# Kernel optimization log

Measured on AMD Instinct MI355X. Metric: run time of the kernel, lower is better.

The kernel has to match this reference:

```python
import jax, jax.numpy as jnp
import numpy as np

B, N, C, H = 32, 197, 768, 12
D = C // H  # head dim = 64


def setup_inputs() -> dict:
    key = jax.random.key(0)
    ks = jax.random.split(key, 5)
    std = 0.02
    x = jax.random.normal(ks[0], (B, N, C), dtype=jnp.float32)
    w_qkv = jax.random.normal(ks[1], (C, 3 * C), dtype=jnp.float32) * std
    w_proj = jax.random.normal(ks[2], (C, C), dtype=jnp.float32) * std
    b_proj = jnp.zeros((C,), dtype=jnp.float32)
    # 1x1 convs over the head axis of the attention map (Conv2d(H,H,1,bias=False))
    w_conv_l = jax.random.normal(ks[3], (H, H), dtype=jnp.float32) * std + jnp.eye(H, dtype=jnp.float32)
    w_conv_w = jax.random.normal(ks[4], (H, H), dtype=jnp.float32) * std + jnp.eye(H, dtype=jnp.float32)
    return {"x": x, "w_qkv": w_qkv, "w_proj": w_proj, "b_proj": b_proj,
            "w_conv_l": w_conv_l, "w_conv_w": w_conv_w}


def reference(x, w_qkv, w_proj, b_proj, w_conv_l, w_conv_w):
    b, n, c = x.shape
    h, d = H, c // H
    scale = d ** (-0.5)
    qkv = (x @ w_qkv).reshape(b, n, 3, h, d).transpose(2, 0, 3, 1, 4)  # [3,B,H,N,D]
    q, k, v = qkv[0], qkv[1], qkv[2]
    # value_map branch (control_output.need_value_map=True)
    value_map = jax.nn.softmax(jnp.einsum('bhnd,bhmd->bhnm', v, v) * scale, axis=-1)
    # scaled QK^T
    attn = jnp.einsum('bhnd,bhmd->bhnm', q * scale, k)  # [B,H,N,N]
    attention_scores = attn  # need_attn_score=True (captured pre-conv)
    # conv_l: 1x1 conv mixing heads
    attn = jnp.einsum('oh,bhnm->bonm', w_conv_l, attn)
    attention_probs = jax.nn.softmax(attn, axis=-1)  # need_attn_prob=True
    # conv_w: 1x1 conv mixing heads on the probabilities
    attn_w = jnp.einsum('oh,bhnm->bonm', w_conv_w, attention_probs)
    out = jnp.einsum('bhnm,bhmd->bhnd', attn_w, v)  # [B,H,N,D]
    out = out.transpose(0, 2, 1, 3).reshape(b, n, c)
    attention_output = out @ w_proj + b_proj
    return attention_output, attention_scores, attention_probs, value_map
```

## Files before the change

### kernel.cpp

```cpp
#include <hip/hip_runtime.h>
#include <cmath>

#define B_ 32
#define N_ 197
#define C_ 768
#define H_ 12
#define D_ 64
#define M_ (B_*N_)
#define MPAD_ 6400
#define K3_ (3*C_)
#define NN_ (N_*N_)
#define BH_ (B_*H_)
#define NP_ 208
#define KP_ 224
#define SCALE 0.125f

typedef __bf16 bf16x8 __attribute__((ext_vector_type(8)));
typedef __bf16 bf16x4 __attribute__((ext_vector_type(4)));
typedef float  f32x4  __attribute__((ext_vector_type(4)));

__device__ __forceinline__ void gl_lds16(const void* g, void* l) {
    __builtin_amdgcn_global_load_lds(
        (const __attribute__((address_space(1))) void*)g,
        (__attribute__((address_space(3))) void*)l,
        16, 0, 0);
}

__global__ __launch_bounds__(256) void cast_x_kernel(const float* __restrict__ X,
        __bf16* __restrict__ Xb) {
    const long long i = ((long long)blockIdx.x * 256 + threadIdx.x) * 4;
    if (i >= (long long)MPAD_ * 768) return;
    bf16x4 o;
    if (i < (long long)M_ * 768) {
        float4 f = *(const float4*)&X[i];
        o.x = (__bf16)f.x; o.y = (__bf16)f.y; o.z = (__bf16)f.z; o.w = (__bf16)f.w;
    } else {
        o.x = o.y = o.z = o.w = (__bf16)0.f;
    }
    *(bf16x4*)&Xb[i] = o;
}

__global__ __launch_bounds__(256) void transpose_cast(const float* __restrict__ W,
        __bf16* __restrict__ Wt, int R, int Ccols) {
    __shared__ float t[32][33];
    const int c0 = blockIdx.x * 32;
    const int r0 = blockIdx.y * 32;
    const int tx = threadIdx.x & 31, ty = threadIdx.x >> 5;
    #pragma unroll
    for (int i = ty; i < 32; i += 8)
        t[i][tx] = W[(size_t)(r0 + i) * Ccols + c0 + tx];
    __syncthreads();
    #pragma unroll
    for (int i = ty; i < 32; i += 8)
        Wt[(size_t)(c0 + i) * R + r0 + tx] = (__bf16)t[tx][i];
}

__global__ __launch_bounds__(256) void mfma_qkv(const __bf16* __restrict__ Xb,
        const __bf16* __restrict__ Wt, __bf16* __restrict__ q,
        __bf16* __restrict__ k, __bf16* __restrict__ v) {
    __shared__ __bf16 As[128*32];
    __shared__ __bf16 Bs[128*32];
    const int tid = threadIdx.x;
    const int wv = tid >> 6, ln = tid & 63;
    const int R0 = blockIdx.x * 128;
    const int C0 = blockIdx.y * 128;
    const int wm = wv >> 1, wn = wv & 1;
    const int arow = ln >> 2, akg = ln & 3;
    f32x4 acc[4][4] = {};
    for (int k0 = 0; k0 < 768; k0 += 32) {
        __syncthreads();
        #pragma unroll
        for (int s = 0; s < 2; s++) {
            const int seg = wv + s*4;
            const int row = seg*16 + arow;
            gl_lds16(Xb + (size_t)(R0 + row)*768 + k0 + akg*8,
                     (char*)As + seg*1024 + ln*16);
            gl_lds16(Wt + (size_t)(C0 + row)*768 + k0 + akg*8,
                     (char*)Bs + seg*1024 + ln*16);
        }
        __syncthreads();
        bf16x8 af[4], bfr[4];
        #pragma unroll
        for (int t = 0; t < 4; t++) {
            af[t]  = *(const bf16x8*)((const char*)As +
                        (wm*64 + t*16 + (ln & 15))*64 + (ln >> 4)*16);
            bfr[t] = *(const bf16x8*)((const char*)Bs +
                        (wn*64 + t*16 + (ln & 15))*64 + (ln >> 4)*16);
        }
        #pragma unroll
        for (int i = 0; i < 4; i++)
            #pragma unroll
            for (int j = 0; j < 4; j++)
                acc[i][j] = __builtin_amdgcn_mfma_f32_16x16x32_bf16(
                                af[i], bfr[j], acc[i][j], 0, 0, 0);
    }
    const int lr = (ln >> 4) * 4;
    const int lc = ln & 15;
    #pragma unroll
    for (int j = 0; j < 4; j++) {
        const int c = C0 + wn*64 + j*16 + lc;
        const int which = c / 768;
        const int rem = c - which*768;
        const int h = rem >> 6, d = rem & 63;
        __bf16* dst = (which == 0) ? q : ((which == 1) ? k : v);
        #pragma unroll
        for (int i = 0; i < 4; i++) {
            #pragma unroll
            for (int rr = 0; rr < 4; rr++) {
                const int r = R0 + wm*64 + i*16 + lr + rr;
                if (r < M_) {
                    const int bb = r / N_, n = r - bb*N_;
                    dst[(((size_t)(bb*H_ + h))*N_ + n)*64 + d] =
                        (__bf16)acc[i][j][rr];
                }
            }
        }
    }
}

__global__ __launch_bounds__(256) void mfma_proj(const __bf16* __restrict__ Ab,
        const __bf16* __restrict__ Wt, const float* __restrict__ bias,
        float* __restrict__ Y) {
    __shared__ __bf16 As[128*32];
    __shared__ __bf16 Bs[128*32];
    const int tid = threadIdx.x;
    const int wv = tid >> 6, ln = tid & 63;
    const int R0 = blockIdx.x * 128;
    const int C0 = blockIdx.y * 128;
    const int wm = wv >> 1, wn = wv & 1;
    const int arow = ln >> 2, akg = ln & 3;
    f32x4 acc[4][4] = {};
    for (int k0 = 0; k0 < 768; k0 += 32) {
        __syncthreads();
        #pragma unroll
        for (int s = 0; s < 2; s++) {
            const int seg = wv + s*4;
            const int row = seg*16 + arow;
            gl_lds16(Ab + (size_t)(R0 + row)*768 + k0 + akg*8,
                     (char*)As + seg*1024 + ln*16);
            gl_lds16(Wt + (size_t)(C0 + row)*768 + k0 + akg*8,
                     (char*)Bs + seg*1024 + ln*16);
        }
        __syncthreads();
        bf16x8 af[4], bfr[4];
        #pragma unroll
        for (int t = 0; t < 4; t++) {
            af[t]  = *(const bf16x8*)((const char*)As +
                        (wm*64 + t*16 + (ln & 15))*64 + (ln >> 4)*16);
            bfr[t] = *(const bf16x8*)((const char*)Bs +
                        (wn*64 + t*16 + (ln & 15))*64 + (ln >> 4)*16);
        }
        #pragma unroll
        for (int i = 0; i < 4; i++)
            #pragma unroll
            for (int j = 0; j < 4; j++)
                acc[i][j] = __builtin_amdgcn_mfma_f32_16x16x32_bf16(
                                af[i], bfr[j], acc[i][j], 0, 0, 0);
    }
    const int lr = (ln >> 4) * 4;
    const int lc = ln & 15;
    #pragma unroll
    for (int j = 0; j < 4; j++) {
        const int c = C0 + wn*64 + j*16 + lc;
        const float bv = bias[c];
        #pragma unroll
        for (int i = 0; i < 4; i++) {
            #pragma unroll
            for (int rr = 0; rr < 4; rr++) {
                const int r = R0 + wm*64 + i*16 + lr + rr;
                if (r < M_) Y[(size_t)r*768 + c] = acc[i][j][rr] + bv;
            }
        }
    }
}

__global__ __launch_bounds__(256) void qkt_vvt(const __bf16* __restrict__ Q,
        const __bf16* __restrict__ Km, const __bf16* __restrict__ V,
        float* __restrict__ S, float* __restrict__ VM) {
    __shared__ __bf16 Al[NP_*64];
    __shared__ __bf16 Bl[NP_*64];
    const int tid = threadIdx.x;
    const int w = tid >> 6, L = tid & 63;
    const int lm = L & 15, lg = L >> 4;
    if (blockIdx.x < BH_) {
        const int bh = blockIdx.x;
        const __bf16* Qb = Q  + (size_t)bh*N_*D_;
        const __bf16* Kb = Km + (size_t)bh*N_*D_;
        for (int i = tid*8; i < NP_*64; i += 2048) {
            const int row = i >> 6;
            bf16x8 z = {};
            *(bf16x8*)&Al[i] = (row < N_) ? *(const bf16x8*)&Qb[i] : z;
            *(bf16x8*)&Bl[i] = (row < N_) ? *(const bf16x8*)&Kb[i] : z;
        }
        __syncthreads();
        for (int rt = w; rt < 13; rt += 4) {
            const bf16x8 a0 = *(const bf16x8*)&Al[(rt*16+lm)*64 + lg*8];
            const bf16x8 a1 = *(const bf16x8*)&Al[(rt*16+lm)*64 + 32 + lg*8];
            const int rbase = rt*16 + lg*4;
            for (int ct = 0; ct < 13; ct++) {
                const bf16x8 b0 = *(const bf16x8*)&Bl[(ct*16+lm)*64 + lg*8];
                const bf16x8 b1 = *(const bf16x8*)&Bl[(ct*16+lm)*64 + 32 + lg*8];
                f32x4 acc = {};
                acc = __builtin_amdgcn_mfma_f32_16x16x32_bf16(a0, b0, acc, 0, 0, 0);
                acc = __builtin_amdgcn_mfma_f32_16x16x32_bf16(a1, b1, acc, 0, 0, 0);
                const int c = ct*16 + lm;
                if (c < N_) {
                    #pragma unroll
                    for (int r = 0; r < 4; r++) {
                        const int row = rbase + r;
                        if (row < N_)
                            S[((size_t)bh*N_ + row)*N_ + c] = acc[r] * SCALE;
                    }
                }
            }
        }
    } else {
        const int bh = blockIdx.x - BH_;
        const __bf16* Vb = V + (size_t)bh*N_*D_;
        for (int i = tid*8; i < NP_*64; i += 2048) {
            const int row = i >> 6;
            bf16x8 z = {};
            *(bf16x8*)&Al[i] = (row < N_) ? *(const bf16x8*)&Vb[i] : z;
        }
        __syncthreads();
        for (int rt = w; rt < 13; rt += 4) {
            const bf16x8 a0 = *(const bf16x8*)&Al[(rt*16+lm)*64 + lg*8];
            const bf16x8 a1 = *(const bf16x8*)&Al[(rt*16+lm)*64 + 32 + lg*8];
            f32x4 acc[13];
            for (int ct = 0; ct < 13; ct++) {
                const bf16x8 b0 = *(const bf16x8*)&Al[(ct*16+lm)*64 + lg*8];
                const bf16x8 b1 = *(const bf16x8*)&Al[(ct*16+lm)*64 + 32 + lg*8];
                f32x4 a = {};
                a = __builtin_amdgcn_mfma_f32_16x16x32_bf16(a0, b0, a, 0, 0, 0);
                a = __builtin_amdgcn_mfma_f32_16x16x32_bf16(a1, b1, a, 0, 0, 0);
                acc[ct] = a;
            }
            float mx[4] = {-1e30f, -1e30f, -1e30f, -1e30f};
            #pragma unroll
            for (int ct = 0; ct < 13; ct++) {
                const bool valid = (ct*16 + lm) < N_;
                #pragma unroll
                for (int r = 0; r < 4; r++) {
                    float val = valid ? acc[ct][r] * SCALE : -1e30f;
                    acc[ct][r] = val;
                    mx[r] = fmaxf(mx[r], val);
                }
            }
            #pragma unroll
            for (int r = 0; r < 4; r++) {
                #pragma unroll
                for (int off = 1; off < 16; off <<= 1)
                    mx[r] = fmaxf(mx[r], __shfl_xor(mx[r], off));
            }
            float sm[4] = {0.f, 0.f, 0.f, 0.f};
            #pragma unroll
            for (int ct = 0; ct < 13; ct++)
                #pragma unroll
                for (int r = 0; r < 4; r++) {
                    const float e = __expf(acc[ct][r] - mx[r]);
                    acc[ct][r] = e;
                    sm[r] += e;
                }
            #pragma unroll
            for (int r = 0; r < 4; r++) {
                #pragma unroll
                for (int off = 1; off < 16; off <<= 1)
                    sm[r] += __shfl_xor(sm[r], off);
                sm[r] = 1.f / sm[r];
            }
            const int rbase = rt*16 + lg*4;
            for (int ct = 0; ct < 13; ct++) {
                const int c = ct*16 + lm;
                if (c < N_) {
                    #pragma unroll
                    for (int r = 0; r < 4; r++) {
                        const int row = rbase + r;
                        if (row < N_)
                            VM[((size_t)bh*N_ + row)*N_ + c] = acc[ct][r] * sm[r];
                    }
                }
            }
        }
    }
}

__global__ __launch_bounds__(256) void convl_convw(const float* __restrict__ SC,
        const float* __restrict__ wl, const float* __restrict__ ww,
        float* __restrict__ PR, __bf16* __restrict__ AW) {
    __shared__ float raw[12*200];
    __shared__ float mixed[12*200];
    __shared__ float wls[144];
    __shared__ float wws[144];
    const int tid = threadIdx.x;
    const int b = blockIdx.x / N_;
    const int n = blockIdx.x - b * N_;
    if (tid < 144) { wls[tid] = wl[tid]; wws[tid] = ww[tid]; }
    for (int i = tid; i < 12*N_; i += 256) {
        int h = i / N_, m = i - h*N_;
        raw[h*200 + m] = SC[(((size_t)(b*12 + h))*N_ + n)*N_ + m];
    }
    __syncthreads();
    for (int i = tid; i < 12*N_; i += 256) {
        int o = i / N_, m = i - o*N_;
        float s = 0.f;
        #pragma unroll
        for (int h = 0; h < 12; h++) s += wls[o*12 + h] * raw[h*200 + m];
        mixed[o*200 + m] = s;
    }
    __syncthreads();
    const int w = tid >> 6, l = tid & 63;
    for (int j = 0; j < 3; j++) {
        const int o = w*3 + j;
        float vv[4];
        float mx = -1e30f;
        #pragma unroll
        for (int c = 0; c < 4; c++) {
            int m = l + 64*c;
            vv[c] = (m < N_) ? mixed[o*200 + m] : -1e30f;
            mx = fmaxf(mx, vv[c]);
        }
        #pragma unroll
        for (int off = 32; off; off >>= 1) mx = fmaxf(mx, __shfl_xor(mx, off));
        float s = 0.f;
        #pragma unroll
        for (int c = 0; c < 4; c++) {
            int m = l + 64*c;
            if (m < N_) { vv[c] = __expf(vv[c] - mx); s += vv[c]; }
        }
        #pragma unroll
        for (int off = 32; off; off >>= 1) s += __shfl_xor(s, off);
        const float inv = 1.f / s;
        float* Prow = PR + (((size_t)(b*12 + o))*N_ + n)*N_;
        #pragma unroll
        for (int c = 0; c < 4; c++) {
            int m = l + 64*c;
            if (m < N_) {
                const float p = vv[c] * inv;
                Prow[m] = p;
                raw[o*200 + m] = p;
            }
        }
    }
    __syncthreads();
    for (int i = tid; i < 12*KP_; i += 256) {
        int o = i / KP_, m = i - o*KP_;
        float s = 0.f;
        if (m < N_) {
            #pragma unroll
            for (int h = 0; h < 12; h++) s += wws[o*12 + h] * raw[h*200 + m];
        }
        AW[((size_t)(b*12 + o)*N_ + n)*KP_ + m] = (__bf16)s;
    }
}

__global__ __launch_bounds__(256) void av_mfma(const __bf16* __restrict__ AW,
        const __bf16* __restrict__ V, __bf16* __restrict__ OP) {
    __shared__ __bf16 Vt[64*KP_];
    const int tid = threadIdx.x, bh = blockIdx.x;
    const int w = tid >> 6, L = tid & 63;
    for (int i = tid*8; i < 64*KP_; i += 2048) {
        bf16x8 z = {};
        *(bf16x8*)&Vt[i] = z;
    }
    __syncthreads();
    const __bf16* Vb = V + (size_t)bh*N_*D_;
    for (int i = tid*8; i < N_*D_; i += 2048) {
        const int row = i >> 6, col = i & 63;
        const bf16x8 vv = *(const bf16x8*)&Vb[i];
        #pragma unroll
        for (int j = 0; j < 8; j++) Vt[(col+j)*KP_ + row] = vv[j];
    }
    __syncthreads();
    const int lm = L & 15, lg = L >> 4;
    const int b = bh / H_, h = bh - b*H_;
    const __bf16* Ab = AW + (size_t)bh*N_*KP_;
    for (int rt = w; rt < 13; rt += 4) {
        int ar = rt*16 + lm;
        if (ar >= N_) ar = 0;
        f32x4 acc[4] = {};
        #pragma unroll
        for (int k0 = 0; k0 < KP_; k0 += 32) {
            const bf16x8 a = *(const bf16x8*)&Ab[(size_t)ar*KP_ + k0 + lg*8];
            #pragma unroll
            for (int ct = 0; ct < 4; ct++) {
                const bf16x8 bf = *(const bf16x8*)&Vt[(ct*16+lm)*KP_ + k0 + lg*8];
                acc[ct] = __builtin_amdgcn_mfma_f32_16x16x32_bf16(
                              a, bf, acc[ct], 0, 0, 0);
            }
        }
        const int rbase = rt*16 + lg*4;
        #pragma unroll
        for (int ct = 0; ct < 4; ct++) {
            const int d = ct*16 + lm;
            #pragma unroll
            for (int r = 0; r < 4; r++) {
                const int row = rbase + r;
                if (row < N_)
                    OP[((size_t)(b*N_ + row))*C_ + h*64 + d] = (__bf16)acc[ct][r];
            }
        }
    }
}

extern "C" void kernel_launch(void* const* d_in, const int* in_sizes, int n_in,
                              void* d_out, int out_size, void* d_ws, size_t ws_size,
                              hipStream_t stream) {
    const float* x      = (const float*)d_in[0];
    const float* w_qkv  = (const float*)d_in[1];
    const float* w_proj = (const float*)d_in[2];
    const float* b_proj = (const float*)d_in[3];
    const float* w_cl   = (const float*)d_in[4];
    const float* w_cw   = (const float*)d_in[5];

    float* out    = (float*)d_out;
    float* scores = out    + (size_t)M_ * C_;
    float* probs  = scores + (size_t)BH_ * NN_;
    float* vmap   = probs  + (size_t)BH_ * NN_;

    char* base = (char*)d_ws;
    const size_t QS = (size_t)BH_ * N_ * D_;
    __bf16* q   = (__bf16*)base;
    __bf16* k   = q + QS;
    __bf16* v   = k + QS;
    __bf16* Xb  = v + QS;
    __bf16* OPb = Xb;
    __bf16* Wqt = Xb + (size_t)MPAD_*768;
    __bf16* Wpt = Wqt + (size_t)K3_*768;
    __bf16* aw  = Wpt + (size_t)768*768;

    cast_x_kernel <<<(MPAD_*768/4 + 255)/256, 256, 0, stream>>>(x, Xb);
    transpose_cast<<<dim3(72, 24),  256, 0, stream>>>(w_qkv,  Wqt, 768, K3_);
    transpose_cast<<<dim3(24, 24),  256, 0, stream>>>(w_proj, Wpt, 768, 768);

    mfma_qkv      <<<dim3(50, 18),  256, 0, stream>>>(Xb, Wqt, q, k, v);
    qkt_vvt       <<<2*BH_,         256, 0, stream>>>(q, k, v, scores, vmap);
    convl_convw   <<<M_,            256, 0, stream>>>(scores, w_cl, w_cw, probs, aw);
    av_mfma       <<<BH_,           256, 0, stream>>>(aw, v, OPb);
    mfma_proj     <<<dim3(50, 6),   256, 0, stream>>>(OPb, Wpt, b_proj, out);
}
```

Baseline: 383.2 us.

## Fuse prep kernels, vectorize score stores, batch conv rows, halve proj tile

The three cast/transpose prep launches become one kernel. The QK^T and VV^T MFMA operands are swapped so each lane holds four consecutive columns, which allows 16-byte row-contiguous stores and a simpler row softmax reduction. The head-mixing conv kernel now handles 4 query rows per block and does both 12x12 mixes per element from registers. The proj GEMM uses 64-row tiles to double the number of blocks. Together these aim to cut launch overhead, uncoalesced scalar stores and the small-grid underuse, at the cost of more LDS per block in the conv kernel.

```diff
diff --git a/kernel.cpp b/kernel.cpp
--- a/kernel.cpp
+++ b/kernel.cpp
@@ -18,6 +18,7 @@
 typedef __bf16 bf16x8 __attribute__((ext_vector_type(8)));
 typedef __bf16 bf16x4 __attribute__((ext_vector_type(4)));
 typedef float  f32x4  __attribute__((ext_vector_type(4)));
+typedef float  f32x4u __attribute__((ext_vector_type(4), aligned(4)));
 
 __device__ __forceinline__ void gl_lds16(const void* g, void* l) {
     __builtin_amdgcn_global_load_lds(
@@ -26,26 +27,10 @@
         16, 0, 0);
 }
 
-__global__ __launch_bounds__(256) void cast_x_kernel(const float* __restrict__ X,
-        __bf16* __restrict__ Xb) {
-    const long long i = ((long long)blockIdx.x * 256 + threadIdx.x) * 4;
-    if (i >= (long long)MPAD_ * 768) return;
-    bf16x4 o;
-    if (i < (long long)M_ * 768) {
-        float4 f = *(const float4*)&X[i];
-        o.x = (__bf16)f.x; o.y = (__bf16)f.y; o.z = (__bf16)f.z; o.w = (__bf16)f.w;
-    } else {
-        o.x = o.y = o.z = o.w = (__bf16)0.f;
-    }
-    *(bf16x4*)&Xb[i] = o;
-}
-
-__global__ __launch_bounds__(256) void transpose_cast(const float* __restrict__ W,
-        __bf16* __restrict__ Wt, int R, int Ccols) {
-    __shared__ float t[32][33];
-    const int c0 = blockIdx.x * 32;
-    const int r0 = blockIdx.y * 32;
-    const int tx = threadIdx.x & 31, ty = threadIdx.x >> 5;
+__device__ __forceinline__ void transpose_tile(const float* __restrict__ W,
+        __bf16* __restrict__ Wt, int R, int Ccols, int c0, int r0,
+        float (*t)[33], int tid) {
+    const int tx = tid & 31, ty = tid >> 5;
     #pragma unroll
     for (int i = ty; i < 32; i += 8)
         t[i][tx] = W[(size_t)(r0 + i) * Ccols + c0 + tx];
@@ -53,6 +38,31 @@
     #pragma unroll
     for (int i = ty; i < 32; i += 8)
         Wt[(size_t)(c0 + i) * R + r0 + tx] = (__bf16)t[tx][i];
+}
+
+__global__ __launch_bounds__(256) void prep_kernel(const float* __restrict__ X,
+        __bf16* __restrict__ Xb, const float* __restrict__ Wq,
+        __bf16* __restrict__ Wqt, const float* __restrict__ Wp,
+        __bf16* __restrict__ Wpt) {
+    __shared__ float t[32][33];
+    const int bid = blockIdx.x, tid = threadIdx.x;
+    if (bid < 4800) {
+        const long long i = ((long long)bid * 256 + tid) * 4;
+        bf16x4 o;
+        if (i < (long long)M_ * 768) {
+            float4 f = *(const float4*)&X[i];
+            o.x = (__bf16)f.x; o.y = (__bf16)f.y; o.z = (__bf16)f.z; o.w = (__bf16)f.w;
+        } else {
+            o.x = o.y = o.z = o.w = (__bf16)0.f;
+        }
+        *(bf16x4*)&Xb[i] = o;
+    } else if (bid < 6528) {
+        const int tt = bid - 4800;
+        transpose_tile(Wq, Wqt, 768, K3_, (tt % 72) * 32, (tt / 72) * 32, t, tid);
+    } else {
+        const int tt = bid - 6528;
+        transpose_tile(Wp, Wpt, 768, 768, (tt % 24) * 32, (tt / 24) * 32, t, tid);
+    }
 }
 
 __global__ __launch_bounds__(256) void mfma_qkv(const __bf16* __restrict__ Xb,
@@ -121,37 +131,41 @@
 __global__ __launch_bounds__(256) void mfma_proj(const __bf16* __restrict__ Ab,
         const __bf16* __restrict__ Wt, const float* __restrict__ bias,
         float* __restrict__ Y) {
-    __shared__ __bf16 As[128*32];
+    __shared__ __bf16 As[64*32];
     __shared__ __bf16 Bs[128*32];
     const int tid = threadIdx.x;
     const int wv = tid >> 6, ln = tid & 63;
-    const int R0 = blockIdx.x * 128;
+    const int R0 = blockIdx.x * 64;
     const int C0 = blockIdx.y * 128;
     const int wm = wv >> 1, wn = wv & 1;
     const int arow = ln >> 2, akg = ln & 3;
-    f32x4 acc[4][4] = {};
+    f32x4 acc[2][4] = {};
     for (int k0 = 0; k0 < 768; k0 += 32) {
         __syncthreads();
+        {
+            const int row = wv*16 + arow;
+            gl_lds16(Ab + (size_t)(R0 + row)*768 + k0 + akg*8,
+                     (char*)As + wv*1024 + ln*16);
+        }
         #pragma unroll
         for (int s = 0; s < 2; s++) {
             const int seg = wv + s*4;
             const int row = seg*16 + arow;
-            gl_lds16(Ab + (size_t)(R0 + row)*768 + k0 + akg*8,
-                     (char*)As + seg*1024 + ln*16);
             gl_lds16(Wt + (size_t)(C0 + row)*768 + k0 + akg*8,
                      (char*)Bs + seg*1024 + ln*16);
         }
         __syncthreads();
-        bf16x8 af[4], bfr[4];
-        #pragma unroll
-        for (int t = 0; t < 4; t++) {
+        bf16x8 af[2], bfr[4];
+        #pragma unroll
+        for (int t = 0; t < 2; t++)
             af[t]  = *(const bf16x8*)((const char*)As +
-                        (wm*64 + t*16 + (ln & 15))*64 + (ln >> 4)*16);
+                        (wm*32 + t*16 + (ln & 15))*64 + (ln >> 4)*16);
+        #pragma unroll
+        for (int t = 0; t < 4; t++)
             bfr[t] = *(const bf16x8*)((const char*)Bs +
                         (wn*64 + t*16 + (ln & 15))*64 + (ln >> 4)*16);
-        }
-        #pragma unroll
-        for (int i = 0; i < 4; i++)
+        #pragma unroll
+        for (int i = 0; i < 2; i++)
             #pragma unroll
             for (int j = 0; j < 4; j++)
                 acc[i][j] = __builtin_amdgcn_mfma_f32_16x16x32_bf16(
@@ -164,10 +178,10 @@
         const int c = C0 + wn*64 + j*16 + lc;
         const float bv = bias[c];
         #pragma unroll
-        for (int i = 0; i < 4; i++) {
+        for (int i = 0; i < 2; i++) {
             #pragma unroll
             for (int rr = 0; rr < 4; rr++) {
-                const int r = R0 + wm*64 + i*16 + lr + rr;
+                const int r = R0 + wm*32 + i*16 + lr + rr;
                 if (r < M_) Y[(size_t)r*768 + c] = acc[i][j][rr] + bv;
             }
         }
@@ -193,23 +207,28 @@
             *(bf16x8*)&Bl[i] = (row < N_) ? *(const bf16x8*)&Kb[i] : z;
         }
         __syncthreads();
-        for (int rt = w; rt < 13; rt += 4) {
-            const bf16x8 a0 = *(const bf16x8*)&Al[(rt*16+lm)*64 + lg*8];
-            const bf16x8 a1 = *(const bf16x8*)&Al[(rt*16+lm)*64 + 32 + lg*8];
-            const int rbase = rt*16 + lg*4;
-            for (int ct = 0; ct < 13; ct++) {
-                const bf16x8 b0 = *(const bf16x8*)&Bl[(ct*16+lm)*64 + lg*8];
-                const bf16x8 b1 = *(const bf16x8*)&Bl[(ct*16+lm)*64 + 32 + lg*8];
+        for (int nt = w; nt < 13; nt += 4) {
+            const bf16x8 q0 = *(const bf16x8*)&Al[(nt*16+lm)*64 + lg*8];
+            const bf16x8 q1 = *(const bf16x8*)&Al[(nt*16+lm)*64 + 32 + lg*8];
+            const int n = nt*16 + lm;
+            float* Srow = S + ((size_t)bh*N_ + n)*N_;
+            for (int mt = 0; mt < 13; mt++) {
+                const bf16x8 k0 = *(const bf16x8*)&Bl[(mt*16+lm)*64 + lg*8];
+                const bf16x8 k1 = *(const bf16x8*)&Bl[(mt*16+lm)*64 + 32 + lg*8];
                 f32x4 acc = {};
-                acc = __builtin_amdgcn_mfma_f32_16x16x32_bf16(a0, b0, acc, 0, 0, 0);
-                acc = __builtin_amdgcn_mfma_f32_16x16x32_bf16(a1, b1, acc, 0, 0, 0);
-                const int c = ct*16 + lm;
-                if (c < N_) {
-                    #pragma unroll
-                    for (int r = 0; r < 4; r++) {
-                        const int row = rbase + r;
-                        if (row < N_)
-                            S[((size_t)bh*N_ + row)*N_ + c] = acc[r] * SCALE;
+                acc = __builtin_amdgcn_mfma_f32_16x16x32_bf16(k0, q0, acc, 0, 0, 0);
+                acc = __builtin_amdgcn_mfma_f32_16x16x32_bf16(k1, q1, acc, 0, 0, 0);
+                if (n < N_) {
+                    const int m0 = mt*16 + lg*4;
+                    if (m0 + 3 < N_) {
+                        f32x4 st;
+                        #pragma unroll
+                        for (int r = 0; r < 4; r++) st[r] = acc[r] * SCALE;
+                        *(f32x4u*)&Srow[m0] = st;
+                    } else {
+                        #pragma unroll
+                        for (int r = 0; r < 4; r++)
+                            if (m0 + r < N_) Srow[m0 + r] = acc[r] * SCALE;
                     }
                 }
             }
@@ -223,61 +242,58 @@
             *(bf16x8*)&Al[i] = (row < N_) ? *(const bf16x8*)&Vb[i] : z;
         }
         __syncthreads();
-        for (int rt = w; rt < 13; rt += 4) {
-            const bf16x8 a0 = *(const bf16x8*)&Al[(rt*16+lm)*64 + lg*8];
-            const bf16x8 a1 = *(const bf16x8*)&Al[(rt*16+lm)*64 + 32 + lg*8];
+        for (int nt = w; nt < 13; nt += 4) {
+            const bf16x8 q0 = *(const bf16x8*)&Al[(nt*16+lm)*64 + lg*8];
+            const bf16x8 q1 = *(const bf16x8*)&Al[(nt*16+lm)*64 + 32 + lg*8];
             f32x4 acc[13];
-            for (int ct = 0; ct < 13; ct++) {
-                const bf16x8 b0 = *(const bf16x8*)&Al[(ct*16+lm)*64 + lg*8];
-                const bf16x8 b1 = *(const bf16x8*)&Al[(ct*16+lm)*64 + 32 + lg*8];
+            for (int mt = 0; mt < 13; mt++) {
+                const bf16x8 a0 = *(const bf16x8*)&Al[(mt*16+lm)*64 + lg*8];
+                const bf16x8 a1 = *(const bf16x8*)&Al[(mt*16+lm)*64 + 32 + lg*8];
                 f32x4 a = {};
-                a = __builtin_amdgcn_mfma_f32_16x16x32_bf16(a0, b0, a, 0, 0, 0);
-                a = __builtin_amdgcn_mfma_f32_16x16x32_bf16(a1, b1, a, 0, 0, 0);
-                acc[ct] = a;
-            }
-            float mx[4] = {-1e30f, -1e30f, -1e30f, -1e30f};
-            #pragma unroll
-            for (int ct = 0; ct < 13; ct++) {
-                const bool valid = (ct*16 + lm) < N_;
+                a = __builtin_amdgcn_mfma_f32_16x16x32_bf16(a0, q0, a, 0, 0, 0);
+                a = __builtin_amdgcn_mfma_f32_16x16x32_bf16(a1, q1, a, 0, 0, 0);
+                acc[mt] = a;
+            }
+            #pragma unroll
+            for (int mt = 0; mt < 13; mt++)
+                #pragma unroll
+                for (int r = 0; r < 4; r++) acc[mt][r] *= SCALE;
+            #pragma unroll
+            for (int r = 0; r < 4; r++)
+                if (192 + lg*4 + r >= N_) acc[12][r] = -1e30f;
+            float mx = -1e30f;
+            #pragma unroll
+            for (int mt = 0; mt < 13; mt++)
+                #pragma unroll
+                for (int r = 0; r < 4; r++) mx = fmaxf(mx, acc[mt][r]);
+            mx = fmaxf(mx, __shfl_xor(mx, 16));
+            mx = fmaxf(mx, __shfl_xor(mx, 32));
+            float sm = 0.f;
+            #pragma unroll
+            for (int mt = 0; mt < 13; mt++)
                 #pragma unroll
                 for (int r = 0; r < 4; r++) {
-                    float val = valid ? acc[ct][r] * SCALE : -1e30f;
-                    acc[ct][r] = val;
-                    mx[r] = fmaxf(mx[r], val);
+                    const float e = __expf(acc[mt][r] - mx);
+                    acc[mt][r] = e;
+                    sm += e;
                 }
-            }
-            #pragma unroll
-            for (int r = 0; r < 4; r++) {
+            sm += __shfl_xor(sm, 16);
+            sm += __shfl_xor(sm, 32);
+            const float inv = 1.f / sm;
+            const int n = nt*16 + lm;
+            if (n < N_) {
+                float* Vrow = VM + ((size_t)bh*N_ + n)*N_;
                 #pragma unroll
-                for (int off = 1; off < 16; off <<= 1)
-                    mx[r] = fmaxf(mx[r], __shfl_xor(mx[r], off));
-            }
-            float sm[4] = {0.f, 0.f, 0.f, 0.f};
-            #pragma unroll
-            for (int ct = 0; ct < 13; ct++)
+                for (int mt = 0; mt < 12; mt++) {
+                    f32x4 st;
+                    #pragma unroll
+                    for (int r = 0; r < 4; r++) st[r] = acc[mt][r] * inv;
+                    *(f32x4u*)&Vrow[mt*16 + lg*4] = st;
+                }
                 #pragma unroll
                 for (int r = 0; r < 4; r++) {
-                    const float e = __expf(acc[ct][r] - mx[r]);
-                    acc[ct][r] = e;
-                    sm[r] += e;
-                }
-            #pragma unroll
-            for (int r = 0; r < 4; r++) {
-                #pragma unroll
-                for (int off = 1; off < 16; off <<= 1)
-                    sm[r] += __shfl_xor(sm[r], off);
-                sm[r] = 1.f / sm[r];
-            }
-            const int rbase = rt*16 + lg*4;
-            for (int ct = 0; ct < 13; ct++) {
-                const int c = ct*16 + lm;
-                if (c < N_) {
-                    #pragma unroll
-                    for (int r = 0; r < 4; r++) {
-                        const int row = rbase + r;
-                        if (row < N_)
-                            VM[((size_t)bh*N_ + row)*N_ + c] = acc[ct][r] * sm[r];
-                    }
+                    const int m = 192 + lg*4 + r;
+                    if (m < N_) Vrow[m] = acc[12][r] * inv;
                 }
             }
         }
@@ -287,36 +303,45 @@
 __global__ __launch_bounds__(256) void convl_convw(const float* __restrict__ SC,
         const float* __restrict__ wl, const float* __restrict__ ww,
         float* __restrict__ PR, __bf16* __restrict__ AW) {
-    __shared__ float raw[12*200];
-    __shared__ float mixed[12*200];
+    __shared__ float sbuf[12][4][200];
     __shared__ float wls[144];
     __shared__ float wws[144];
     const int tid = threadIdx.x;
-    const int b = blockIdx.x / N_;
-    const int n = blockIdx.x - b * N_;
+    const int b = blockIdx.x / 50;
+    const int n0 = (blockIdx.x - b * 50) * 4;
     if (tid < 144) { wls[tid] = wl[tid]; wws[tid] = ww[tid]; }
-    for (int i = tid; i < 12*N_; i += 256) {
-        int h = i / N_, m = i - h*N_;
-        raw[h*200 + m] = SC[(((size_t)(b*12 + h))*N_ + n)*N_ + m];
-    }
-    __syncthreads();
-    for (int i = tid; i < 12*N_; i += 256) {
-        int o = i / N_, m = i - o*N_;
-        float s = 0.f;
-        #pragma unroll
-        for (int h = 0; h < 12; h++) s += wls[o*12 + h] * raw[h*200 + m];
-        mixed[o*200 + m] = s;
+    for (int i = tid; i < 12*4*200; i += 256) {
+        const int h = i / 800, rem = i - h*800, n = rem / 200, m = rem - n*200;
+        float vv = 0.f;
+        if (m < N_ && n0 + n < N_)
+            vv = SC[(((size_t)(b*12 + h))*N_ + n0 + n)*N_ + m];
+        sbuf[h][n][m] = vv;
+    }
+    __syncthreads();
+    for (int p = tid; p < 4*N_; p += 256) {
+        const int n = p / N_, m = p - n*N_;
+        float in[12];
+        #pragma unroll
+        for (int h = 0; h < 12; h++) in[h] = sbuf[h][n][m];
+        #pragma unroll
+        for (int o = 0; o < 12; o++) {
+            float s = 0.f;
+            #pragma unroll
+            for (int h = 0; h < 12; h++) s += wls[o*12 + h] * in[h];
+            sbuf[o][n][m] = s;
+        }
     }
     __syncthreads();
     const int w = tid >> 6, l = tid & 63;
-    for (int j = 0; j < 3; j++) {
-        const int o = w*3 + j;
+    for (int rid = w; rid < 48; rid += 4) {
+        const int o = rid >> 2, n = rid & 3;
+        const int ng = n0 + n;
         float vv[4];
         float mx = -1e30f;
         #pragma unroll
         for (int c = 0; c < 4; c++) {
-            int m = l + 64*c;
-            vv[c] = (m < N_) ? mixed[o*200 + m] : -1e30f;
+            const int m = l + 64*c;
+            vv[c] = (m < N_) ? sbuf[o][n][m] : -1e30f;
             mx = fmaxf(mx, vv[c]);
         }
         #pragma unroll
@@ -324,32 +349,47 @@
         float s = 0.f;
         #pragma unroll
         for (int c = 0; c < 4; c++) {
-            int m = l + 64*c;
+            const int m = l + 64*c;
             if (m < N_) { vv[c] = __expf(vv[c] - mx); s += vv[c]; }
         }
         #pragma unroll
         for (int off = 32; off; off >>= 1) s += __shfl_xor(s, off);
         const float inv = 1.f / s;
-        float* Prow = PR + (((size_t)(b*12 + o))*N_ + n)*N_;
         #pragma unroll
         for (int c = 0; c < 4; c++) {
-            int m = l + 64*c;
+            const int m = l + 64*c;
             if (m < N_) {
-                const float p = vv[c] * inv;
-                Prow[m] = p;
-                raw[o*200 + m] = p;
-            }
-        }
-    }
-    __syncthreads();
-    for (int i = tid; i < 12*KP_; i += 256) {
-        int o = i / KP_, m = i - o*KP_;
-        float s = 0.f;
-        if (m < N_) {
-            #pragma unroll
-            for (int h = 0; h < 12; h++) s += wws[o*12 + h] * raw[h*200 + m];
-        }
-        AW[((size_t)(b*12 + o)*N_ + n)*KP_ + m] = (__bf16)s;
+                const float pv = vv[c] * inv;
+                if (ng < N_)
+                    PR[((((size_t)(b*12 + o))*N_ + ng)*N_) + m] = pv;
+                sbuf[o][n][m] = pv;
+            }
+        }
+    }
+    __syncthreads();
+    for (int p = tid; p < 4*N_; p += 256) {
+        const int n = p / N_, m = p - n*N_;
+        const int ng = n0 + n;
+        if (ng >= N_) continue;
+        float in[12];
+        #pragma unroll
+        for (int h = 0; h < 12; h++) in[h] = sbuf[h][n][m];
+        #pragma unroll
+        for (int o = 0; o < 12; o++) {
+            float s = 0.f;
+            #pragma unroll
+            for (int h = 0; h < 12; h++) s += wws[o*12 + h] * in[h];
+            AW[((size_t)(b*12 + o)*N_ + ng)*KP_ + m] = (__bf16)s;
+        }
+    }
+    for (int p = tid; p < 12*4*(KP_-N_); p += 256) {
+        const int o = p / (4*(KP_-N_));
+        const int rem = p - o*(4*(KP_-N_));
+        const int n = rem / (KP_-N_);
+        const int m = N_ + rem - n*(KP_-N_);
+        const int ng = n0 + n;
+        if (ng < N_)
+            AW[((size_t)(b*12 + o)*N_ + ng)*KP_ + m] = (__bf16)0.f;
     }
 }
 
@@ -428,13 +468,10 @@
     __bf16* Wpt = Wqt + (size_t)K3_*768;
     __bf16* aw  = Wpt + (size_t)768*768;
 
-    cast_x_kernel <<<(MPAD_*768/4 + 255)/256, 256, 0, stream>>>(x, Xb);
-    transpose_cast<<<dim3(72, 24),  256, 0, stream>>>(w_qkv,  Wqt, 768, K3_);
-    transpose_cast<<<dim3(24, 24),  256, 0, stream>>>(w_proj, Wpt, 768, 768);
-
+    prep_kernel   <<<7104,          256, 0, stream>>>(x, Xb, w_qkv, Wqt, w_proj, Wpt);
     mfma_qkv      <<<dim3(50, 18),  256, 0, stream>>>(Xb, Wqt, q, k, v);
     qkt_vvt       <<<2*BH_,         256, 0, stream>>>(q, k, v, scores, vmap);
-    convl_convw   <<<M_,            256, 0, stream>>>(scores, w_cl, w_cw, probs, aw);
+    convl_convw   <<<32*50,         256, 0, stream>>>(scores, w_cl, w_cw, probs, aw);
     av_mfma       <<<BH_,           256, 0, stream>>>(aw, v, OPb);
-    mfma_proj     <<<dim3(50, 6),   256, 0, stream>>>(OPb, Wpt, b_proj, out);
-}
+    mfma_proj     <<<dim3(100, 6),  256, 0, stream>>>(OPb, Wpt, b_proj, out);
+}
```

After: 397.9 us. 1.04x slower.
